# Optimization experiments

Measured on AMD Instinct MI355X. Metric: run time of the kernel, lower is better.

Reference implementation:

```python
import jax, jax.numpy as jnp
import numpy as np

D = 512          # d_model
DS = 32          # d_state
EXPAND = 2
HEADDIM = 64
R = 4            # mimo_rank
DIN = EXPAND * D             # 1024 inner dim
H = DIN // HEADDIM           # 16 heads
DFF = ((int(D * 8 / 3) + 7) // 8) * 8  # 1368 SwiGLU hidden
CHUNK = max(1, 64 // R)      # 16
BATCH, SEQ = 4, 512


def setup_inputs() -> dict:
    key = jax.random.key(0)
    ks = jax.random.split(key, 12)
    def w(k, shape, fan):
        return jax.random.normal(k, shape, jnp.float32) / np.float32(np.sqrt(fan))
    return {
        "x": jax.random.normal(ks[0], (BATCH, SEQ, D), jnp.float32),
        "mask": jnp.ones((BATCH, SEQ), jnp.float32),
        "norm1_w": jnp.ones((D,), jnp.float32),
        "norm2_w": jnp.ones((D,), jnp.float32),
        "Wz": w(ks[1], (D, DIN), D),
        "Wx": w(ks[2], (D, DIN), D),
        "Wb": w(ks[3], (D, H * R * DS), D),
        "Wc": w(ks[4], (D, H * R * DS), D),
        "Wdt": w(ks[5], (D, H), D),
        "dt_bias": jnp.zeros((H,), jnp.float32),
        "A_log": jnp.log(jnp.arange(1, H + 1, dtype=jnp.float32)),
        "D_skip": jnp.ones((H,), jnp.float32),
        "Wout": w(ks[6], (DIN, D), DIN),
        "w1": w(ks[7], (D, DFF), D),
        "w2": w(ks[8], (DFF, D), DFF),
        "w3": w(ks[9], (D, DFF), D),
    }


def rmsnorm(x, wgt, eps=1e-6):
    rms = jnp.sqrt(jnp.mean(x * x, axis=-1, keepdims=True) + eps)
    return x / rms * wgt


def ssm_mixer(x, Wz, Wx, Wb, Wc, Wdt, dt_bias, A_log, D_skip, Wout):
    # x: [B, S, D] (already masked)
    B, S, _ = x.shape
    pad = (CHUNK - S % CHUNK) % CHUNK
    if pad > 0:
        x = jnp.pad(x, ((0, 0), (0, pad), (0, 0)))
    Sp = x.shape[1]
    z = x @ Wz                                        # [B,Sp,DIN] gate
    u = (x @ Wx).reshape(B, Sp, H, HEADDIM)           # [B,Sp,H,P]
    Bm = (x @ Wb).reshape(B, Sp, H, R, DS)            # [B,Sp,H,R,N]
    Cm = (x @ Wc).reshape(B, Sp, H, R, DS)
    dt = jax.nn.softplus(x @ Wdt + dt_bias)           # [B,Sp,H]
    a = jnp.exp(dt * (-jnp.exp(A_log)))               # per-step decay [B,Sp,H]
    ud = u * dt[..., None]                            # discretized input

    def step(h, inp):
        a_t, B_t, C_t, ud_t = inp                     # [B,H], [B,H,R,N], [B,H,R,N], [B,H,P]
        h = a_t[:, :, None, None, None] * h + jnp.einsum('bhrn,bhp->bhrnp', B_t, ud_t)
        y = jnp.einsum('bhrn,bhrnp->bhp', C_t, h)
        return h, y

    h0 = jnp.zeros((B, H, R, DS, HEADDIM), x.dtype)
    xs = (a.swapaxes(0, 1), Bm.swapaxes(0, 1), Cm.swapaxes(0, 1), ud.swapaxes(0, 1))
    _, ys = jax.lax.scan(step, h0, xs)                # ys: [Sp,B,H,P]
    y = ys.swapaxes(0, 1) + u * D_skip[None, None, :, None]
    y = y.reshape(B, Sp, DIN) * jax.nn.silu(z)
    y = y @ Wout                                      # [B,Sp,D]
    return y[:, :S]


def reference(x, mask, norm1_w, norm2_w, Wz, Wx, Wb, Wc, Wdt, dt_bias,
              A_log, D_skip, Wout, w1, w2, w3):
    m = mask[..., None]
    xn = rmsnorm(x, norm1_w) * m
    y = ssm_mixer(xn, Wz, Wx, Wb, Wc, Wdt, dt_bias, A_log, D_skip, Wout) * m
    x = x + y
    xn2 = rmsnorm(x, norm2_w)
    x = x + (jax.nn.silu(xn2 @ w1) * (xn2 @ w3)) @ w2
    return x * m
```

## Files before the change

kernel.cpp:

```cpp
#include <hip/hip_runtime.h>
#include <hip/hip_bf16.h>
#include <math.h>

#define Bn 4
#define Sn 512
#define Dn 512
#define DINn 1024
#define Hn 16
#define Pn 64
#define RNn 128
#define DFFn 1368
#define KP2 1408
#define BSn (Bn*Sn)
#define CH 64
#define NCH (Sn/CH)
#define PSTR 6144
#define FPAD 2816
#define NSCAN (Bn*NCH*Hn)

typedef __attribute__((ext_vector_type(8))) short short8;
typedef __attribute__((ext_vector_type(4))) float f32x4;
typedef __attribute__((ext_vector_type(4))) short short4v;

static __device__ __forceinline__ float bf2f(__hip_bfloat16 v){return __bfloat162float(v);}
static __device__ __forceinline__ __hip_bfloat16 f2bf(float v){return __float2bfloat16(v);}
static __device__ __forceinline__ short f2bfs(float v){ __hip_bfloat16 b=f2bf(v); short s; __builtin_memcpy(&s,&b,2); return s; }
static __device__ __forceinline__ float bfs2f(short s){ __hip_bfloat16 b; __builtin_memcpy(&b,&s,2); return bf2f(b); }

typedef const __attribute__((address_space(1))) unsigned int* gas1_u32p;
typedef __attribute__((address_space(3))) unsigned int* gas3_u32p;
static __device__ __forceinline__ void gl_lds16(const void* g, void* l) {
  __builtin_amdgcn_global_load_lds((gas1_u32p)g, (gas3_u32p)l, 16, 0, 0);
}

struct T8 {
  const float* src[8];
  __hip_bfloat16* dst[8];
  int Rr[8], Cc[8], RrPad[8], CcPad[8], gw[8];
  int start[9];
};

static __device__ __forceinline__ void transpose_tile(const T8& d, int bid, int t,
                                                      float (*tile)[65]) {
  int i = 0;
#pragma unroll
  for (int k = 1; k < 8; ++k) if (bid >= d.start[k]) i = k;
  int rel = bid - d.start[i];
  int gx = rel % d.gw[i], gy = rel / d.gw[i];
  const float* in = d.src[i];
  __hip_bfloat16* out = d.dst[i];
  int Rr = d.Rr[i], Cc = d.Cc[i], RrPad = d.RrPad[i], CcPad = d.CcPad[i];
  int tx = t & 15, ty = t >> 4;
#pragma unroll
  for (int i4 = 0; i4 < 4; ++i4) {
    int r = gy * 64 + ty + i4 * 16;
    int c0 = gx * 64 + tx * 4;
    f32x4 v = (f32x4){0.f, 0.f, 0.f, 0.f};
    if (r < Rr && c0 + 3 < Cc) v = *(const f32x4*)(in + (size_t)r * Cc + c0);
    tile[ty + i4 * 16][tx * 4 + 0] = v[0];
    tile[ty + i4 * 16][tx * 4 + 1] = v[1];
    tile[ty + i4 * 16][tx * 4 + 2] = v[2];
    tile[ty + i4 * 16][tx * 4 + 3] = v[3];
  }
  __syncthreads();
#pragma unroll
  for (int i4 = 0; i4 < 4; ++i4) {
    int r2 = gx * 64 + ty + i4 * 16;
    int c2 = gy * 64 + tx * 4;
    if (r2 < CcPad && c2 + 3 < RrPad) {
      int k = ty + i4 * 16;
      short4v o;
      o.x = f2bfs(tile[tx * 4 + 0][k]);
      o.y = f2bfs(tile[tx * 4 + 1][k]);
      o.z = f2bfs(tile[tx * 4 + 2][k]);
      o.w = f2bfs(tile[tx * 4 + 3][k]);
      *(short4v*)((short*)out + (size_t)r2 * RrPad + c2) = o;
    }
  }
}

__global__ __launch_bounds__(256) void prep_kernel(
    T8 d, const float* __restrict__ x, const float* __restrict__ w,
    const float* __restrict__ mask, const float* __restrict__ Wdt,
    const float* __restrict__ dtb, const float* __restrict__ Alog,
    __hip_bfloat16* __restrict__ outb, float* __restrict__ dt,
    float* __restrict__ la, float* __restrict__ rs, int tstart) {
  __shared__ float tile[64][65];
  __shared__ float xs[Dn];
  __shared__ float red[4];
  int bid = blockIdx.x, t = threadIdx.x;
  if (bid < tstart) {
    transpose_tile(d, bid, t, tile);
  } else if (bid - tstart < BSn) {
    int row = bid - tstart;
    const float* xr = x + (size_t)row * Dn;
    float v0 = xr[t], v1 = xr[t + 256];
    float ss = v0 * v0 + v1 * v1;
#pragma unroll
    for (int o = 32; o > 0; o >>= 1) ss += __shfl_down(ss, o);
    if ((t & 63) == 0) red[t >> 6] = ss;
    __syncthreads();
    float tot = red[0] + red[1] + red[2] + red[3];
    float sc = rsqrtf(tot * (1.f / Dn) + 1e-6f) * mask[row];
    float o0 = v0 * sc * w[t], o1v = v1 * sc * w[t + 256];
    outb[(size_t)row * Dn + t] = f2bf(o0);
    outb[(size_t)row * Dn + t + 256] = f2bf(o1v);
    xs[t] = o0;
    xs[t + 256] = o1v;
    __syncthreads();
    int h = t >> 4, j = t & 15;
    float s = 0.f;
#pragma unroll
    for (int kk = 0; kk < 32; ++kk) {
      int k = j + kk * 16;
      s = fmaf(xs[k], Wdt[k * Hn + h], s);
    }
#pragma unroll
    for (int o = 8; o > 0; o >>= 1) s += __shfl_down(s, o, 16);
    if (j == 0) {
      float v = s + dtb[h];
      float sp = (v > 20.f) ? v : log1pf(expf(v));
      float Ah = expf(Alog[h]);
      dt[(size_t)row * Hn + h] = sp;
      la[(size_t)row * Hn + h] = -Ah * sp;
    }
  } else {
    *(f32x4*)&rs[t * 8]     = (f32x4){0.f, 0.f, 0.f, 0.f};
    *(f32x4*)&rs[t * 8 + 4] = (f32x4){0.f, 0.f, 0.f, 0.f};
  }
}

__global__ __launch_bounds__(256) void gemm_kernel(
    const __hip_bfloat16* __restrict__ A, const __hip_bfloat16* __restrict__ BT,
    __hip_bfloat16* __restrict__ C, int M, int N, int K) {
  __shared__ short As[2][4096];
  __shared__ short Bs[2][4096];
  int m0 = blockIdx.x * 128, n0 = blockIdx.y * 128;
  int t = threadIdx.x;
  int lane = t & 63, wv = t >> 6;
  int wm = (wv & 1) * 64, wn = (wv >> 1) * 64;
  f32x4 acc[4][4];
#pragma unroll
  for (int i = 0; i < 4; ++i)
#pragma unroll
    for (int j = 0; j < 4; ++j) acc[i][j] = (f32x4){0.f, 0.f, 0.f, 0.f};
  const short* Ag = (const short*)A;
  const short* Bg = (const short*)BT;
  int r0 = t >> 2, p = t & 3;
  int q0 = (p - (r0 >> 1)) & 3;
  int r1 = r0 + 64;
  int q1 = (p - (r1 >> 1)) & 3;
  const short* Asrc0 = Ag + (size_t)(m0 + r0) * K + 8 * q0;
  const short* Asrc1 = Ag + (size_t)(m0 + r1) * K + 8 * q1;
  const short* Bsrc0 = Bg + (size_t)(n0 + r0) * K + 8 * q0;
  const short* Bsrc1 = Bg + (size_t)(n0 + r1) * K + 8 * q1;
  int fr = lane & 15, fq = lane >> 4;
  int kTiles = K >> 5;
  auto stage = [&](int buf, int k0) {
    gl_lds16(Asrc0 + k0, &As[buf][wv * 512]);
    gl_lds16(Asrc1 + k0, &As[buf][2048 + wv * 512]);
    gl_lds16(Bsrc0 + k0, &Bs[buf][wv * 512]);
    gl_lds16(Bsrc1 + k0, &Bs[buf][2048 + wv * 512]);
  };
  auto domfma = [&](int buf) {
    short8 af[4], bfr[4];
#pragma unroll
    for (int i = 0; i < 4; ++i) {
      int rr = wm + i * 16 + fr;
      af[i] = *(const short8*)&As[buf][rr * 32 + (((rr >> 1) + fq) & 3) * 8];
    }
#pragma unroll
    for (int i = 0; i < 4; ++i) {
      int rr = wn + i * 16 + fr;
      bfr[i] = *(const short8*)&Bs[buf][rr * 32 + (((rr >> 1) + fq) & 3) * 8];
    }
#pragma unroll
    for (int mi = 0; mi < 4; ++mi)
#pragma unroll
      for (int ni = 0; ni < 4; ++ni)
        acc[mi][ni] = __builtin_amdgcn_mfma_f32_16x16x32_bf16(af[mi], bfr[ni], acc[mi][ni], 0, 0, 0);
  };
  stage(0, 0);
  for (int kt = 0; kt < kTiles; ++kt) {
    int buf = kt & 1;
    __syncthreads();
    if (kt + 1 < kTiles) stage(buf ^ 1, (kt + 1) << 5);
    domfma(buf);
  }
  int fq4 = (lane >> 4) * 4;
#pragma unroll
  for (int mi = 0; mi < 4; ++mi)
#pragma unroll
    for (int ni = 0; ni < 4; ++ni) {
      int col = n0 + wn + ni * 16 + fr;
      if (col < N) {
        int rowb = m0 + wm + mi * 16 + fq4;
#pragma unroll
        for (int r = 0; r < 4; ++r)
          C[(size_t)(rowb + r) * N + col] = f2bf(acc[mi][ni][r]);
      }
    }
}

template <int MODE>
__global__ __launch_bounds__(256) void gemm64_ep_kernel(
    const __hip_bfloat16* __restrict__ A, const __hip_bfloat16* __restrict__ BT,
    const float* __restrict__ aux, const float* __restrict__ mask,
    float* __restrict__ out, float* __restrict__ rs, int M, int N, int K) {
  __shared__ short As[2][64][72];
  __shared__ short Bs[2][64][72];
  int m0 = blockIdx.x * 64, n0 = blockIdx.y * 64;
  int t = threadIdx.x;
  int lane = t & 63, wv = t >> 6;
  int wm = (wv & 1) * 32, wn = (wv >> 1) * 32;
  f32x4 acc[2][2];
#pragma unroll
  for (int i = 0; i < 2; ++i)
#pragma unroll
    for (int j = 0; j < 2; ++j) acc[i][j] = (f32x4){0.f, 0.f, 0.f, 0.f};
  const short* Ag = (const short*)A;
  const short* Bg = (const short*)BT;
  int sr = t >> 2;
  int sc = (t & 3) * 16;
  const short* Ap = Ag + (size_t)(m0 + sr) * K + sc;
  const short* Bp = Bg + (size_t)(n0 + sr) * K + sc;
  int fr = lane & 15, fq = (lane >> 4) * 8;
  int kTiles = K >> 6;
  short8 a0A = 0, a1A = 0, b0A = 0, b1A = 0;
  short8 a0B = 0, a1B = 0, b0B = 0, b1B = 0;
  auto loadA = [&](int k0) {
    a0A = *(const short8*)(Ap + k0);
    a1A = *(const short8*)(Ap + k0 + 8);
    b0A = *(const short8*)(Bp + k0);
    b1A = *(const short8*)(Bp + k0 + 8);
  };
  auto loadB = [&](int k0) {
    a0B = *(const short8*)(Ap + k0);
    a1B = *(const short8*)(Ap + k0 + 8);
    b0B = *(const short8*)(Bp + k0);
    b1B = *(const short8*)(Bp + k0 + 8);
  };
  auto storeA = [&](int buf) {
    *(short8*)&As[buf][sr][sc] = a0A;
    *(short8*)&As[buf][sr][sc + 8] = a1A;
    *(short8*)&Bs[buf][sr][sc] = b0A;
    *(short8*)&Bs[buf][sr][sc + 8] = b1A;
  };
  auto storeB = [&](int buf) {
    *(short8*)&As[buf][sr][sc] = a0B;
    *(short8*)&As[buf][sr][sc + 8] = a1B;
    *(short8*)&Bs[buf][sr][sc] = b0B;
    *(short8*)&Bs[buf][sr][sc + 8] = b1B;
  };
  auto mfma = [&](int buf) {
#pragma unroll
    for (int kk = 0; kk < 2; ++kk) {
      short8 af[2], bfr[2];
#pragma unroll
      for (int i = 0; i < 2; ++i) af[i] = *(const short8*)&As[buf][wm + i * 16 + fr][kk * 32 + fq];
#pragma unroll
      for (int i = 0; i < 2; ++i) bfr[i] = *(const short8*)&Bs[buf][wn + i * 16 + fr][kk * 32 + fq];
#pragma unroll
      for (int mi = 0; mi < 2; ++mi)
#pragma unroll
        for (int ni = 0; ni < 2; ++ni)
          acc[mi][ni] = __builtin_amdgcn_mfma_f32_16x16x32_bf16(af[mi], bfr[ni], acc[mi][ni], 0, 0, 0);
    }
  };
  loadA(0);
  storeA(0);
  loadA(64);
  __syncthreads();
  for (int kt = 0; kt < kTiles; kt += 2) {
    storeA(1);
    if (kt + 2 < kTiles) loadB((kt + 2) << 6);
    mfma(0);
    __syncthreads();
    if (kt + 2 < kTiles) storeB(0);
    if (kt + 3 < kTiles) loadA((kt + 3) << 6);
    mfma(1);
    __syncthreads();
  }
  int fq4 = (lane >> 4) * 4;
  float rsum[2][4];
#pragma unroll
  for (int mi = 0; mi < 2; ++mi)
#pragma unroll
    for (int r = 0; r < 4; ++r) rsum[mi][r] = 0.f;
#pragma unroll
  for (int mi = 0; mi < 2; ++mi)
#pragma unroll
    for (int ni = 0; ni < 2; ++ni) {
      int col = n0 + wn + ni * 16 + fr;
#pragma unroll
      for (int r = 0; r < 4; ++r) {
        int row = m0 + wm + mi * 16 + fq4 + r;
        float m = mask[row];
        size_t a = (size_t)row * N + col;
        float v = acc[mi][ni][r];
        if (MODE == 1) {
          float ov = aux[a] + v * m;
          out[a] = ov;
          rsum[mi][r] += ov * ov;
        } else {
          out[a] = (aux[a] + v) * m;
        }
      }
    }
  if (MODE == 1) {
#pragma unroll
    for (int mi = 0; mi < 2; ++mi)
#pragma unroll
      for (int r = 0; r < 4; ++r) {
        float s = rsum[mi][r];
#pragma unroll
        for (int o = 8; o > 0; o >>= 1) s += __shfl_xor(s, o);
        if ((lane & 15) == 0) {
          int row = m0 + wm + mi * 16 + fq4 + r;
          atomicAdd(&rs[row], s);
        }
      }
  }
}

__global__ __launch_bounds__(256) void gemm64g_kernel(
    const float* __restrict__ X, const float* __restrict__ rs,
    const float* __restrict__ n2w, const __hip_bfloat16* __restrict__ BT,
    __hip_bfloat16* __restrict__ G, int M, int K) {
  __shared__ short As[2][64][72];
  __shared__ short B1s[2][64][72];
  __shared__ short B3s[2][64][72];
  __shared__ float ssc[64];
  __shared__ float sw[Dn];
  int m0 = blockIdx.x * 64, n0 = blockIdx.y * 64;
  int t = threadIdx.x;
  int lane = t & 63, wv = t >> 6;
  int wm = (wv & 1) * 32, wn = (wv >> 1) * 32;
  f32x4 acc1[2][2], acc3[2][2];
#pragma unroll
  for (int i = 0; i < 2; ++i)
#pragma unroll
    for (int j = 0; j < 2; ++j) {
      acc1[i][j] = (f32x4){0.f, 0.f, 0.f, 0.f};
      acc3[i][j] = (f32x4){0.f, 0.f, 0.f, 0.f};
    }
  const short* Bg = (const short*)BT;
  int sr = t >> 2;
  int sc = (t & 3) * 16;
  const float* Xp  = X + (size_t)(m0 + sr) * Dn + sc;
  const short* B1p = Bg + (size_t)(n0 + sr) * K + sc;
  const short* B3p = Bg + (size_t)(DFFn + n0 + sr) * K + sc;
  int fr = lane & 15, fq = (lane >> 4) * 8;
  int kTiles = K >> 6;
  if (t < 64) ssc[t] = rsqrtf(rs[m0 + t] * (1.f / Dn) + 1e-6f);
  sw[t] = n2w[t];
  sw[t + 256] = n2w[t + 256];
  __syncthreads();
  float scl = ssc[sr];
  short8 a0A = 0, a1A = 0, c0A = 0, c1A = 0, d0A = 0, d1A = 0;
  short8 a0B = 0, a1B = 0, c0B = 0, c1B = 0, d0B = 0, d1B = 0;
  auto cvtA = [&](int k0, short8& lo, short8& hi) {
    f32x4 v[4];
#pragma unroll
    for (int q = 0; q < 4; ++q) v[q] = *(const f32x4*)(Xp + k0 + q * 4);
    short tmp[16];
#pragma unroll
    for (int q = 0; q < 4; ++q)
#pragma unroll
      for (int jj = 0; jj < 4; ++jj)
        tmp[q * 4 + jj] = f2bfs(v[q][jj] * scl * sw[k0 + sc + q * 4 + jj]);
    __builtin_memcpy(&lo, tmp, 16);
    __builtin_memcpy(&hi, tmp + 8, 16);
  };
  auto loadA = [&](int k0) {
    cvtA(k0, a0A, a1A);
    c0A = *(const short8*)(B1p + k0);
    c1A = *(const short8*)(B1p + k0 + 8);
    d0A = *(const short8*)(B3p + k0);
    d1A = *(const short8*)(B3p + k0 + 8);
  };
  auto loadB = [&](int k0) {
    cvtA(k0, a0B, a1B);
    c0B = *(const short8*)(B1p + k0);
    c1B = *(const short8*)(B1p + k0 + 8);
    d0B = *(const short8*)(B3p + k0);
    d1B = *(const short8*)(B3p + k0 + 8);
  };
  auto storeA = [&](int buf) {
    *(short8*)&As[buf][sr][sc] = a0A;
    *(short8*)&As[buf][sr][sc + 8] = a1A;
    *(short8*)&B1s[buf][sr][sc] = c0A;
    *(short8*)&B1s[buf][sr][sc + 8] = c1A;
    *(short8*)&B3s[buf][sr][sc] = d0A;
    *(short8*)&B3s[buf][sr][sc + 8] = d1A;
  };
  auto storeB = [&](int buf) {
    *(short8*)&As[buf][sr][sc] = a0B;
    *(short8*)&As[buf][sr][sc + 8] = a1B;
    *(short8*)&B1s[buf][sr][sc] = c0B;
    *(short8*)&B1s[buf][sr][sc + 8] = c1B;
    *(short8*)&B3s[buf][sr][sc] = d0B;
    *(short8*)&B3s[buf][sr][sc + 8] = d1B;
  };
  auto mfma = [&](int buf) {
#pragma unroll
    for (int kk = 0; kk < 2; ++kk) {
      short8 af[2], b1f[2], b3f[2];
#pragma unroll
      for (int i = 0; i < 2; ++i) af[i]  = *(const short8*)&As[buf][wm + i * 16 + fr][kk * 32 + fq];
#pragma unroll
      for (int i = 0; i < 2; ++i) b1f[i] = *(const short8*)&B1s[buf][wn + i * 16 + fr][kk * 32 + fq];
#pragma unroll
      for (int i = 0; i < 2; ++i) b3f[i] = *(const short8*)&B3s[buf][wn + i * 16 + fr][kk * 32 + fq];
#pragma unroll
      for (int mi = 0; mi < 2; ++mi)
#pragma unroll
        for (int ni = 0; ni < 2; ++ni) {
          acc1[mi][ni] = __builtin_amdgcn_mfma_f32_16x16x32_bf16(af[mi], b1f[ni], acc1[mi][ni], 0, 0, 0);
          acc3[mi][ni] = __builtin_amdgcn_mfma_f32_16x16x32_bf16(af[mi], b3f[ni], acc3[mi][ni], 0, 0, 0);
        }
    }
  };
  loadA(0);
  storeA(0);
  loadA(64);
  __syncthreads();
  for (int kt = 0; kt < kTiles; kt += 2) {
    storeA(1);
    if (kt + 2 < kTiles) loadB((kt + 2) << 6);
    mfma(0);
    __syncthreads();
    if (kt + 2 < kTiles) storeB(0);
    if (kt + 3 < kTiles) loadA((kt + 3) << 6);
    mfma(1);
    __syncthreads();
  }
  int fq4 = (lane >> 4) * 4;
#pragma unroll
  for (int mi = 0; mi < 2; ++mi)
#pragma unroll
    for (int ni = 0; ni < 2; ++ni) {
      int col = n0 + wn + ni * 16 + fr;
      bool valid = col < DFFn;
#pragma unroll
      for (int r = 0; r < 4; ++r) {
        int row = m0 + wm + mi * 16 + fq4 + r;
        float h1v = acc1[mi][ni][r];
        float sil = h1v / (1.f + __expf(-h1v));
        float g = sil * acc3[mi][ni][r];
        G[(size_t)row * KP2 + col] = valid ? f2bf(g) : f2bf(0.f);
      }
    }
}

__global__ __launch_bounds__(256) void chunk_intra_kernel(
    const __hip_bfloat16* __restrict__ P, const float* __restrict__ dt,
    const float* __restrict__ la, __hip_bfloat16* __restrict__ ysb,
    __hip_bfloat16* __restrict__ Sbuf, float* __restrict__ ecL, float* __restrict__ ec) {
  int id = blockIdx.x;
  int h = id & 15, c = (id >> 4) & 7, b = id >> 7;
  int t = threadIdx.x, lane = t & 63, wv = t >> 6;
  __shared__ __align__(16) char smem[55040];
  short* sCB = (short*)smem;
  short* sB  = (short*)(smem + 18432);
  short* sUD = (short*)(smem + 35840);
  short* sG  = (short*)(smem + 45056);
  float* scum = (float*)(smem + 54272);
  float* sws  = scum + 64;
  float* sdt  = sws + 64;
  int row0 = b * Sn + c * CH;
  const short* Pb = (const short*)P;
#pragma unroll
  for (int i = 0; i < 4; ++i) {
    int idx = t + i * 256;
    int r = idx >> 4, kk = (idx & 15) * 8;
    *(short8*)&sCB[r * 136 + kk] = *(const short8*)(Pb + (size_t)(row0 + r) * PSTR + 4096 + h * 128 + kk);
    *(short8*)&sB [r * 136 + kk] = *(const short8*)(Pb + (size_t)(row0 + r) * PSTR + 2048 + h * 128 + kk);
  }
  if (t < 64) { sdt[t] = dt[(size_t)(row0 + t) * Hn + h]; scum[t] = la[(size_t)(row0 + t) * Hn + h]; }
  __syncthreads();
  if (wv == 0) {
    float v = scum[lane];
#pragma unroll
    for (int o = 1; o < 64; o <<= 1) { float n = __shfl_up(v, o); if (lane >= o) v += n; }
    scum[lane] = v;
    float c63 = __shfl(v, 63);
    sws[lane] = __expf(c63 - v);
    ec[((size_t)((b * NCH + c) * Hn + h)) * 64 + lane] = __expf(v);
    if (lane == 0) ecL[(b * NCH + c) * Hn + h] = __expf(c63);
  }
#pragma unroll
  for (int i = 0; i < 2; ++i) {
    int idx = t + i * 256;
    int s = idx >> 3, pc = (idx & 7) * 8;
    short8 uv = *(const short8*)(Pb + (size_t)(row0 + s) * PSTR + 1024 + h * 64 + pc);
    float dv = sdt[s];
#pragma unroll
    for (int j = 0; j < 8; ++j) sUD[(pc + j) * 72 + s] = f2bfs(bfs2f(uv[j]) * dv);
  }
  __syncthreads();
  int fr = lane & 15, fq = (lane >> 4) * 8, q4 = (lane >> 4) * 4;
  {
    short8 af[4];
#pragma unroll
    for (int k = 0; k < 4; ++k) af[k] = *(short8*)&sCB[(16 * wv + fr) * 136 + k * 32 + fq];
#pragma unroll
    for (int j = 0; j < 4; ++j) {
      f32x4 acc = (f32x4){0.f, 0.f, 0.f, 0.f};
#pragma unroll
      for (int k = 0; k < 4; ++k) {
        short8 bf = *(short8*)&sB[(16 * j + fr) * 136 + k * 32 + fq];
        acc = __builtin_amdgcn_mfma_f32_16x16x32_bf16(af[k], bf, acc, 0, 0, 0);
      }
      int ss = 16 * j + fr;
      float cs = scum[ss];
#pragma unroll
      for (int r = 0; r < 4; ++r) {
        int tt = 16 * wv + q4 + r;
        float w = (ss <= tt) ? __expf(scum[tt] - cs) : 0.f;
        sG[tt * 72 + ss] = f2bfs(acc[r] * w);
      }
    }
  }
  __syncthreads();
#pragma unroll
  for (int i = 0; i < 32; ++i) {
    int idx = t + i * 256;
    int rn = idx >> 6, s = idx & 63;
    sCB[rn * 72 + s] = f2bfs(bfs2f(sB[s * 136 + rn]) * sws[s]);
  }
  __syncthreads();
  {
    short8 ag[2];
#pragma unroll
    for (int k = 0; k < 2; ++k) ag[k] = *(short8*)&sG[(16 * wv + fr) * 72 + k * 32 + fq];
#pragma unroll
    for (int j = 0; j < 4; ++j) {
      f32x4 acc = (f32x4){0.f, 0.f, 0.f, 0.f};
#pragma unroll
      for (int k = 0; k < 2; ++k) {
        short8 bf = *(short8*)&sUD[(16 * j + fr) * 72 + k * 32 + fq];
        acc = __builtin_amdgcn_mfma_f32_16x16x32_bf16(ag[k], bf, acc, 0, 0, 0);
      }
#pragma unroll
      for (int r = 0; r < 4; ++r)
        ysb[(size_t)(row0 + 16 * wv + q4 + r) * DINn + h * 64 + 16 * j + fr] = f2bf(acc[r]);
    }
  }
#pragma unroll
  for (int mt0 = 0; mt0 < 2; ++mt0) {
    int mt = wv * 2 + mt0;
    short8 ab[2];
#pragma unroll
    for (int k = 0; k < 2; ++k) ab[k] = *(short8*)&sCB[(16 * mt + fr) * 72 + k * 32 + fq];
#pragma unroll
    for (int j = 0; j < 4; ++j) {
      f32x4 acc = (f32x4){0.f, 0.f, 0.f, 0.f};
#pragma unroll
      for (int k = 0; k < 2; ++k) {
        short8 bf = *(short8*)&sUD[(16 * j + fr) * 72 + k * 32 + fq];
        acc = __builtin_amdgcn_mfma_f32_16x16x32_bf16(ab[k], bf, acc, 0, 0, 0);
      }
      int pp = 16 * j + fr;
      int rn0 = 16 * mt + q4;
      short4v o;
      o.x = f2bfs(acc[0]); o.y = f2bfs(acc[1]); o.z = f2bfs(acc[2]); o.w = f2bfs(acc[3]);
      *(short4v*)&((short*)Sbuf)[((size_t)((b * NCH + c) * Hn + h) * 64 + pp) * 128 + rn0] = o;
    }
  }
}

__global__ __launch_bounds__(256) void inter_gate_kernel(
    const __hip_bfloat16* __restrict__ P, const __hip_bfloat16* __restrict__ Sbuf,
    const float* __restrict__ ecL, const float* __restrict__ ec,
    const __hip_bfloat16* __restrict__ ysb, const float* __restrict__ Dsk,
    __hip_bfloat16* __restrict__ y2b) {
  int id = blockIdx.x;
  int h = id & 15, c = (id >> 4) & 7, b = id >> 7;
  int t = threadIdx.x, lane = t & 63, wv = t >> 6;
  __shared__ __align__(16) short sC[64 * 136];
  __shared__ __align__(16) short sHt[64 * 136];
  __shared__ __align__(16) short sz[64 * 64];
  __shared__ __align__(16) short su[64 * 64];
  __shared__ float sec[64];
  int row0 = b * Sn + c * CH;
  const short* Pb = (const short*)P;
#pragma unroll
  for (int i = 0; i < 2; ++i) {
    int idx = t + i * 256;
    int r = idx >> 3, pc = (idx & 7) * 8;
    *(short8*)&sz[r * 64 + pc] = *(const short8*)(Pb + (size_t)(row0 + r) * PSTR + h * 64 + pc);
    *(short8*)&su[r * 64 + pc] = *(const short8*)(Pb + (size_t)(row0 + r) * PSTR + 1024 + h * 64 + pc);
  }
  if (c > 0) {
#pragma unroll
    for (int i = 0; i < 4; ++i) {
      int idx = t + i * 256;
      int r = idx >> 4, kk = (idx & 15) * 8;
      *(short8*)&sC[r * 136 + kk] = *(const short8*)(Pb + (size_t)(row0 + r) * PSTR + 4096 + h * 128 + kk);
    }
    float wch[8];
    {
      float w = 1.f;
      for (int cp = c - 1; cp >= 0; --cp) {
        wch[cp] = w;
        if (cp > 0) w *= ecL[(size_t)((b * NCH + cp) * Hn + h)];
      }
    }
    float hacc[32];
#pragma unroll
    for (int jj = 0; jj < 32; ++jj) hacc[jj] = 0.f;
    const short* Sb = (const short*)Sbuf;
    for (int cp = 0; cp < c; ++cp) {
      size_t base = ((size_t)((b * NCH + cp) * Hn + h)) * 8192 + (size_t)t * 32;
      float wv2 = wch[cp];
#pragma unroll
      for (int v4 = 0; v4 < 4; ++v4) {
        short8 sv = *(const short8*)(Sb + base + v4 * 8);
#pragma unroll
        for (int jj = 0; jj < 8; ++jj)
          hacc[v4 * 8 + jj] = fmaf(wv2, bfs2f(sv[jj]), hacc[v4 * 8 + jj]);
      }
    }
    int p = t >> 2, rn0 = (t & 3) * 32;
#pragma unroll
    for (int v4 = 0; v4 < 4; ++v4) {
      short8 o;
#pragma unroll
      for (int jj = 0; jj < 8; ++jj) o[jj] = f2bfs(hacc[v4 * 8 + jj]);
      *(short8*)&sHt[p * 136 + rn0 + v4 * 8] = o;
    }
    if (t < 64) sec[t] = ec[((size_t)((b * NCH + c) * Hn + h)) * 64 + t];
  }
  __syncthreads();
  int fr = lane & 15, fq = (lane >> 4) * 8, q4 = (lane >> 4) * 4;
  f32x4 acc[4];
#pragma unroll
  for (int j = 0; j < 4; ++j) acc[j] = (f32x4){0.f, 0.f, 0.f, 0.f};
  if (c > 0) {
    short8 af[4];
#pragma unroll
    for (int k = 0; k < 4; ++k) af[k] = *(short8*)&sC[(16 * wv + fr) * 136 + k * 32 + fq];
#pragma unroll
    for (int j = 0; j < 4; ++j)
#pragma unroll
      for (int k = 0; k < 4; ++k) {
        short8 bf = *(short8*)&sHt[(16 * j + fr) * 136 + k * 32 + fq];
        acc[j] = __builtin_amdgcn_mfma_f32_16x16x32_bf16(af[k], bf, acc[j], 0, 0, 0);
      }
  }
  float dsk = Dsk[h];
#pragma unroll
  for (int j = 0; j < 4; ++j) {
    int col = 16 * j + fr;
#pragma unroll
    for (int r = 0; r < 4; ++r) {
      int tt = 16 * wv + q4 + r;
      size_t a = (size_t)(row0 + tt) * DINn + h * 64 + col;
      float val = bf2f(ysb[a]);
      if (c > 0) val += sec[tt] * acc[j][r];
      float uu = bfs2f(su[tt * 64 + col]);
      float zz = bfs2f(sz[tt * 64 + col]);
      float sil = zz / (1.f + __expf(-zz));
      y2b[a] = f2bf((val + uu * dsk) * sil);
    }
  }
}

extern "C" void kernel_launch(void* const* d_in, const int* in_sizes, int n_in,
                              void* d_out, int out_size, void* d_ws, size_t ws_size,
                              hipStream_t stream) {
  const float* x    = (const float*)d_in[0];
  const float* mask = (const float*)d_in[1];
  const float* n1w  = (const float*)d_in[2];
  const float* n2w  = (const float*)d_in[3];
  const float* Wz   = (const float*)d_in[4];
  const float* Wx   = (const float*)d_in[5];
  const float* Wb   = (const float*)d_in[6];
  const float* Wc   = (const float*)d_in[7];
  const float* Wdt  = (const float*)d_in[8];
  const float* dtb  = (const float*)d_in[9];
  const float* Alog = (const float*)d_in[10];
  const float* Dsk  = (const float*)d_in[11];
  const float* Wout = (const float*)d_in[12];
  const float* w1   = (const float*)d_in[13];
  const float* w2   = (const float*)d_in[14];
  const float* w3   = (const float*)d_in[15];

  char* ws = (char*)d_ws;
  size_t off = 0;
  auto alloc = [&](size_t bytes) {
    char* p = ws + off;
    off += (bytes + 255) & ~(size_t)255;
    return p;
  };
  __hip_bfloat16* xnb = (__hip_bfloat16*)alloc((size_t)BSn * Dn * 2);
  __hip_bfloat16* P = (__hip_bfloat16*)alloc((size_t)BSn * PSTR * 2);
  float* dt  = (float*)alloc((size_t)BSn * Hn * 4);
  float* la  = (float*)alloc((size_t)BSn * Hn * 4);
  __hip_bfloat16* ysb = (__hip_bfloat16*)alloc((size_t)BSn * DINn * 2);
  float* ecL = (float*)alloc((size_t)Bn * NCH * Hn * 4);
  float* ec  = (float*)alloc((size_t)Bn * NCH * Hn * 64 * 4);
  float* rs  = (float*)alloc((size_t)BSn * 4);
  __hip_bfloat16* WallT = (__hip_bfloat16*)alloc((size_t)PSTR * Dn * 2);
  __hip_bfloat16* WoutT = (__hip_bfloat16*)alloc((size_t)Dn * DINn * 2);
  __hip_bfloat16* w13T  = (__hip_bfloat16*)alloc((size_t)FPAD * Dn * 2);
  __hip_bfloat16* w2T   = (__hip_bfloat16*)alloc((size_t)Dn * KP2 * 2);
  char* arena = alloc(22000000);
  __hip_bfloat16* Sbuf = (__hip_bfloat16*)arena;
  __hip_bfloat16* y2b  = (__hip_bfloat16*)(arena + 16777216);
  float* xres          = (float*)arena;
  __hip_bfloat16* gatedb = (__hip_bfloat16*)(arena + 4194304);

  T8 td;
  td.src[0] = Wz;   td.dst[0] = WallT;                      td.Rr[0] = 512;  td.Cc[0] = 1024; td.RrPad[0] = 512;  td.CcPad[0] = 1024;
  td.src[1] = Wx;   td.dst[1] = WallT + (size_t)1024 * 512; td.Rr[1] = 512;  td.Cc[1] = 1024; td.RrPad[1] = 512;  td.CcPad[1] = 1024;
  td.src[2] = Wb;   td.dst[2] = WallT + (size_t)2048 * 512; td.Rr[2] = 512;  td.Cc[2] = 2048; td.RrPad[2] = 512;  td.CcPad[2] = 2048;
  td.src[3] = Wc;   td.dst[3] = WallT + (size_t)4096 * 512; td.Rr[3] = 512;  td.Cc[3] = 2048; td.RrPad[3] = 512;  td.CcPad[3] = 2048;
  td.src[4] = Wout; td.dst[4] = WoutT;                      td.Rr[4] = 1024; td.Cc[4] = 512;  td.RrPad[4] = 1024; td.CcPad[4] = 512;
  td.src[5] = w1;   td.dst[5] = w13T;                       td.Rr[5] = 512;  td.Cc[5] = 1368; td.RrPad[5] = 512;  td.CcPad[5] = 1368;
  td.src[6] = w3;   td.dst[6] = w13T + (size_t)1368 * 512;  td.Rr[6] = 512;  td.Cc[6] = 1368; td.RrPad[6] = 512;  td.CcPad[6] = 1448;
  td.src[7] = w2;   td.dst[7] = w2T;                        td.Rr[7] = 1368; td.Cc[7] = 512;  td.RrPad[7] = KP2;  td.CcPad[7] = 512;
  int tot = 0;
  for (int i = 0; i < 8; ++i) {
    td.gw[i] = (td.CcPad[i] + 63) / 64;
    int gh = (td.RrPad[i] + 63) / 64;
    td.start[i] = tot;
    tot += td.gw[i] * gh;
  }
  td.start[8] = tot;

  prep_kernel<<<tot + BSn + 1, 256, 0, stream>>>(td, x, n1w, mask, Wdt, dtb, Alog, xnb, dt, la, rs, tot);
  gemm_kernel<<<dim3(16, 48), 256, 0, stream>>>(xnb, WallT, P, BSn, PSTR, Dn);
  chunk_intra_kernel<<<NSCAN, 256, 0, stream>>>(P, dt, la, ysb, Sbuf, ecL, ec);
  inter_gate_kernel<<<NSCAN, 256, 0, stream>>>(P, Sbuf, ecL, ec, ysb, Dsk, y2b);
  gemm64_ep_kernel<1><<<dim3(32, 8), 256, 0, stream>>>(y2b, WoutT, x, mask, xres, rs, BSn, Dn, DINn);
  gemm64g_kernel<<<dim3(32, KP2 / 64), 256, 0, stream>>>(xres, rs, n2w, w13T, gatedb, BSn, Dn);
  gemm64_ep_kernel<2><<<dim3(32, 8), 256, 0, stream>>>(gatedb, w2T, xres, mask, (float*)d_out, rs, BSn, Dn, KP2);
}
```

Before: 212.6 us.

## Fold norm2 weight into w1/w3 and apply row RMS scale post-GEMM

The norm2 weight is folded into the transposed w1/w3 bf16 weights during prep. The out-projection epilogue also writes a bf16 copy of the residual, so the SwiGLU up-GEMM loads bf16 A directly instead of reading fp32 and converting and scaling it per element. The per-row RMS scale is applied to the accumulators in the epilogue. The inter-chunk state accumulation also computes its decay weights with a running product in a single backward loop, replacing a separate precompute pass. This adds an extra bf16 write in the Wout epilogue, and rounding the unnormalized residual to bf16 before scaling changes numerics slightly.

```diff
diff --git a/kernel.cpp b/kernel.cpp
--- a/kernel.cpp
+++ b/kernel.cpp
@@ -35,6 +35,7 @@
 
 struct T8 {
   const float* src[8];
+  const float* svec[8];
   __hip_bfloat16* dst[8];
   int Rr[8], Cc[8], RrPad[8], CcPad[8], gw[8];
   int start[9];
@@ -48,6 +49,7 @@
   int rel = bid - d.start[i];
   int gx = rel % d.gw[i], gy = rel / d.gw[i];
   const float* in = d.src[i];
+  const float* sv = d.svec[i];
   __hip_bfloat16* out = d.dst[i];
   int Rr = d.Rr[i], Cc = d.Cc[i], RrPad = d.RrPad[i], CcPad = d.CcPad[i];
   int tx = t & 15, ty = t >> 4;
@@ -69,11 +71,15 @@
     int c2 = gy * 64 + tx * 4;
     if (r2 < CcPad && c2 + 3 < RrPad) {
       int k = ty + i4 * 16;
+      float s0 = sv ? sv[c2 + 0] : 1.f;
+      float s1 = sv ? sv[c2 + 1] : 1.f;
+      float s2 = sv ? sv[c2 + 2] : 1.f;
+      float s3 = sv ? sv[c2 + 3] : 1.f;
       short4v o;
-      o.x = f2bfs(tile[tx * 4 + 0][k]);
-      o.y = f2bfs(tile[tx * 4 + 1][k]);
-      o.z = f2bfs(tile[tx * 4 + 2][k]);
-      o.w = f2bfs(tile[tx * 4 + 3][k]);
+      o.x = f2bfs(tile[tx * 4 + 0][k] * s0);
+      o.y = f2bfs(tile[tx * 4 + 1][k] * s1);
+      o.z = f2bfs(tile[tx * 4 + 2][k] * s2);
+      o.w = f2bfs(tile[tx * 4 + 3][k] * s3);
       *(short4v*)((short*)out + (size_t)r2 * RrPad + c2) = o;
     }
   }
@@ -206,7 +212,8 @@
 __global__ __launch_bounds__(256) void gemm64_ep_kernel(
     const __hip_bfloat16* __restrict__ A, const __hip_bfloat16* __restrict__ BT,
     const float* __restrict__ aux, const float* __restrict__ mask,
-    float* __restrict__ out, float* __restrict__ rs, int M, int N, int K) {
+    float* __restrict__ out, __hip_bfloat16* __restrict__ outb,
+    float* __restrict__ rs, int M, int N, int K) {
   __shared__ short As[2][64][72];
   __shared__ short Bs[2][64][72];
   int m0 = blockIdx.x * 64, n0 = blockIdx.y * 64;
@@ -301,6 +308,7 @@
         if (MODE == 1) {
           float ov = aux[a] + v * m;
           out[a] = ov;
+          outb[a] = f2bf(ov);
           rsum[mi][r] += ov * ov;
         } else {
           out[a] = (aux[a] + v) * m;
@@ -324,14 +332,13 @@
 }
 
 __global__ __launch_bounds__(256) void gemm64g_kernel(
-    const float* __restrict__ X, const float* __restrict__ rs,
-    const float* __restrict__ n2w, const __hip_bfloat16* __restrict__ BT,
-    __hip_bfloat16* __restrict__ G, int M, int K) {
+    const __hip_bfloat16* __restrict__ A, const float* __restrict__ rs,
+    const __hip_bfloat16* __restrict__ BT, __hip_bfloat16* __restrict__ G,
+    int M, int K) {
   __shared__ short As[2][64][72];
   __shared__ short B1s[2][64][72];
   __shared__ short B3s[2][64][72];
   __shared__ float ssc[64];
-  __shared__ float sw[Dn];
   int m0 = blockIdx.x * 64, n0 = blockIdx.y * 64;
   int t = threadIdx.x;
   int lane = t & 63, wv = t >> 6;
@@ -344,43 +351,29 @@
       acc1[i][j] = (f32x4){0.f, 0.f, 0.f, 0.f};
       acc3[i][j] = (f32x4){0.f, 0.f, 0.f, 0.f};
     }
+  const short* Ag = (const short*)A;
   const short* Bg = (const short*)BT;
   int sr = t >> 2;
   int sc = (t & 3) * 16;
-  const float* Xp  = X + (size_t)(m0 + sr) * Dn + sc;
+  const short* Ap  = Ag + (size_t)(m0 + sr) * K + sc;
   const short* B1p = Bg + (size_t)(n0 + sr) * K + sc;
   const short* B3p = Bg + (size_t)(DFFn + n0 + sr) * K + sc;
   int fr = lane & 15, fq = (lane >> 4) * 8;
   int kTiles = K >> 6;
   if (t < 64) ssc[t] = rsqrtf(rs[m0 + t] * (1.f / Dn) + 1e-6f);
-  sw[t] = n2w[t];
-  sw[t + 256] = n2w[t + 256];
-  __syncthreads();
-  float scl = ssc[sr];
   short8 a0A = 0, a1A = 0, c0A = 0, c1A = 0, d0A = 0, d1A = 0;
   short8 a0B = 0, a1B = 0, c0B = 0, c1B = 0, d0B = 0, d1B = 0;
-  auto cvtA = [&](int k0, short8& lo, short8& hi) {
-    f32x4 v[4];
-#pragma unroll
-    for (int q = 0; q < 4; ++q) v[q] = *(const f32x4*)(Xp + k0 + q * 4);
-    short tmp[16];
-#pragma unroll
-    for (int q = 0; q < 4; ++q)
-#pragma unroll
-      for (int jj = 0; jj < 4; ++jj)
-        tmp[q * 4 + jj] = f2bfs(v[q][jj] * scl * sw[k0 + sc + q * 4 + jj]);
-    __builtin_memcpy(&lo, tmp, 16);
-    __builtin_memcpy(&hi, tmp + 8, 16);
-  };
   auto loadA = [&](int k0) {
-    cvtA(k0, a0A, a1A);
+    a0A = *(const short8*)(Ap + k0);
+    a1A = *(const short8*)(Ap + k0 + 8);
     c0A = *(const short8*)(B1p + k0);
     c1A = *(const short8*)(B1p + k0 + 8);
     d0A = *(const short8*)(B3p + k0);
     d1A = *(const short8*)(B3p + k0 + 8);
   };
   auto loadB = [&](int k0) {
-    cvtA(k0, a0B, a1B);
+    a0B = *(const short8*)(Ap + k0);
+    a1B = *(const short8*)(Ap + k0 + 8);
     c0B = *(const short8*)(B1p + k0);
     c1B = *(const short8*)(B1p + k0 + 8);
     d0B = *(const short8*)(B3p + k0);
@@ -444,11 +437,12 @@
       bool valid = col < DFFn;
 #pragma unroll
       for (int r = 0; r < 4; ++r) {
-        int row = m0 + wm + mi * 16 + fq4 + r;
-        float h1v = acc1[mi][ni][r];
+        int rloc = wm + mi * 16 + fq4 + r;
+        float scl = ssc[rloc];
+        float h1v = acc1[mi][ni][r] * scl;
         float sil = h1v / (1.f + __expf(-h1v));
-        float g = sil * acc3[mi][ni][r];
-        G[(size_t)row * KP2 + col] = valid ? f2bf(g) : f2bf(0.f);
+        float g = sil * (acc3[mi][ni][r] * scl);
+        G[(size_t)(m0 + rloc) * KP2 + col] = valid ? f2bf(g) : f2bf(0.f);
       }
     }
 }
@@ -599,28 +593,21 @@
       int r = idx >> 4, kk = (idx & 15) * 8;
       *(short8*)&sC[r * 136 + kk] = *(const short8*)(Pb + (size_t)(row0 + r) * PSTR + 4096 + h * 128 + kk);
     }
-    float wch[8];
-    {
-      float w = 1.f;
-      for (int cp = c - 1; cp >= 0; --cp) {
-        wch[cp] = w;
-        if (cp > 0) w *= ecL[(size_t)((b * NCH + cp) * Hn + h)];
-      }
-    }
     float hacc[32];
 #pragma unroll
     for (int jj = 0; jj < 32; ++jj) hacc[jj] = 0.f;
     const short* Sb = (const short*)Sbuf;
-    for (int cp = 0; cp < c; ++cp) {
+    float wrun = 1.f;
+    for (int cp = c - 1; cp >= 0; --cp) {
       size_t base = ((size_t)((b * NCH + cp) * Hn + h)) * 8192 + (size_t)t * 32;
-      float wv2 = wch[cp];
 #pragma unroll
       for (int v4 = 0; v4 < 4; ++v4) {
         short8 sv = *(const short8*)(Sb + base + v4 * 8);
 #pragma unroll
         for (int jj = 0; jj < 8; ++jj)
-          hacc[v4 * 8 + jj] = fmaf(wv2, bfs2f(sv[jj]), hacc[v4 * 8 + jj]);
-      }
+          hacc[v4 * 8 + jj] = fmaf(wrun, bfs2f(sv[jj]), hacc[v4 * 8 + jj]);
+      }
+      wrun *= ecL[(size_t)((b * NCH + cp) * Hn + h)];
     }
     int p = t >> 2, rn0 = (t & 3) * 32;
 #pragma unroll
@@ -706,13 +693,15 @@
   __hip_bfloat16* WoutT = (__hip_bfloat16*)alloc((size_t)Dn * DINn * 2);
   __hip_bfloat16* w13T  = (__hip_bfloat16*)alloc((size_t)FPAD * Dn * 2);
   __hip_bfloat16* w2T   = (__hip_bfloat16*)alloc((size_t)Dn * KP2 * 2);
-  char* arena = alloc(22000000);
+  char* arena = alloc(23200000);
   __hip_bfloat16* Sbuf = (__hip_bfloat16*)arena;
   __hip_bfloat16* y2b  = (__hip_bfloat16*)(arena + 16777216);
   float* xres          = (float*)arena;
   __hip_bfloat16* gatedb = (__hip_bfloat16*)(arena + 4194304);
+  __hip_bfloat16* xresb  = (__hip_bfloat16*)(arena + 20971520);
 
   T8 td;
+  for (int i = 0; i < 8; ++i) td.svec[i] = nullptr;
   td.src[0] = Wz;   td.dst[0] = WallT;                      td.Rr[0] = 512;  td.Cc[0] = 1024; td.RrPad[0] = 512;  td.CcPad[0] = 1024;
   td.src[1] = Wx;   td.dst[1] = WallT + (size_t)1024 * 512; td.Rr[1] = 512;  td.Cc[1] = 1024; td.RrPad[1] = 512;  td.CcPad[1] = 1024;
   td.src[2] = Wb;   td.dst[2] = WallT + (size_t)2048 * 512; td.Rr[2] = 512;  td.Cc[2] = 2048; td.RrPad[2] = 512;  td.CcPad[2] = 2048;
@@ -721,6 +710,8 @@
   td.src[5] = w1;   td.dst[5] = w13T;                       td.Rr[5] = 512;  td.Cc[5] = 1368; td.RrPad[5] = 512;  td.CcPad[5] = 1368;
   td.src[6] = w3;   td.dst[6] = w13T + (size_t)1368 * 512;  td.Rr[6] = 512;  td.Cc[6] = 1368; td.RrPad[6] = 512;  td.CcPad[6] = 1448;
   td.src[7] = w2;   td.dst[7] = w2T;                        td.Rr[7] = 1368; td.Cc[7] = 512;  td.RrPad[7] = KP2;  td.CcPad[7] = 512;
+  td.svec[5] = n2w;
+  td.svec[6] = n2w;
   int tot = 0;
   for (int i = 0; i < 8; ++i) {
     td.gw[i] = (td.CcPad[i] + 63) / 64;
@@ -734,7 +725,7 @@
   gemm_kernel<<<dim3(16, 48), 256, 0, stream>>>(xnb, WallT, P, BSn, PSTR, Dn);
   chunk_intra_kernel<<<NSCAN, 256, 0, stream>>>(P, dt, la, ysb, Sbuf, ecL, ec);
   inter_gate_kernel<<<NSCAN, 256, 0, stream>>>(P, Sbuf, ecL, ec, ysb, Dsk, y2b);
-  gemm64_ep_kernel<1><<<dim3(32, 8), 256, 0, stream>>>(y2b, WoutT, x, mask, xres, rs, BSn, Dn, DINn);
-  gemm64g_kernel<<<dim3(32, KP2 / 64), 256, 0, stream>>>(xres, rs, n2w, w13T, gatedb, BSn, Dn);
-  gemm64_ep_kernel<2><<<dim3(32, 8), 256, 0, stream>>>(gatedb, w2T, xres, mask, (float*)d_out, rs, BSn, Dn, KP2);
-}
+  gemm64_ep_kernel<1><<<dim3(32, 8), 256, 0, stream>>>(y2b, WoutT, x, mask, xres, xresb, rs, BSn, Dn, DINn);
+  gemm64g_kernel<<<dim3(32, KP2 / 64), 256, 0, stream>>>(xresb, rs, w13T, gatedb, BSn, Dn);
+  gemm64_ep_kernel<2><<<dim3(32, 8), 256, 0, stream>>>(gatedb, w2T, xres, mask, (float*)d_out, nullptr, rs, BSn, Dn, KP2);
+}
```

New measurement: 213.9 us. Within noise of the previous version (+0.6%).
